# Kernel tuning notes

Hardware: AMD Instinct MI355X
Metric: run time of the kernel (lower is better)

Reference implementation:

```python
import jax, jax.numpy as jnp
import numpy as np

N_ATOMS = 100000
M_NBRS = 12
ATOM_F = 64
NBR_F = 41
BN_EPS = 1e-5


def setup_inputs() -> dict:
    key = jax.random.key(0)
    k1, k2, k3, k4, k5 = jax.random.split(key, 5)
    atom_fea = jax.random.normal(k1, (N_ATOMS, ATOM_F), dtype=jnp.float32)
    nbr_fea = jax.random.normal(k2, (N_ATOMS, M_NBRS, NBR_F), dtype=jnp.float32)
    # fc_full: Linear(2*atom + nbr -> 2*atom), torch layout [out, in]
    in_dim = 2 * ATOM_F + NBR_F
    out_dim = 2 * ATOM_F
    W = jax.random.normal(k3, (out_dim, in_dim), dtype=jnp.float32) * (1.0 / np.sqrt(in_dim))
    b = jax.random.normal(k4, (out_dim,), dtype=jnp.float32) * 0.01
    gamma = jnp.ones((ATOM_F,), dtype=jnp.float32)
    beta = jnp.zeros((ATOM_F,), dtype=jnp.float32)
    nbr_idx = jax.random.randint(k5, (N_ATOMS, M_NBRS), 0, N_ATOMS, dtype=jnp.int32)
    return {"atom_fea": atom_fea, "nbr_fea": nbr_fea, "W": W, "b": b,
            "gamma": gamma, "beta": beta, "nbr_idx": nbr_idx}


def reference(atom_fea, nbr_fea, W, b, gamma, beta, nbr_idx):
    N, M = nbr_idx.shape
    F = atom_fea.shape[1]
    # gather neighbor atom features: [N, M, F]
    nbr_atom_fea = atom_fea[nbr_idx]
    # broadcast self features: [N, M, F]
    self_fea = jnp.broadcast_to(atom_fea[:, None, :], (N, M, F))
    # concat [self, nbr_atom, edge] -> [N, M, 2F + nbr_F]
    total_fea = jnp.concatenate([self_fea, nbr_atom_fea, nbr_fea], axis=2)
    # shared linear: [N, M, 2F]
    total_fea = jnp.einsum('nmi,oi->nmo', total_fea, W) + b
    filter_fea, core_fea = jnp.split(total_fea, 2, axis=2)
    # gated message, sum over neighbors -> [N, F]
    nbr_msg = (jax.nn.sigmoid(filter_fea) * jax.nn.softplus(core_fea)).sum(axis=1)
    # BatchNorm1d (training mode: batch stats, biased variance)
    x = atom_fea + nbr_msg
    mean = x.mean(axis=0)
    var = x.var(axis=0)
    x_hat = (x - mean) * jax.lax.rsqrt(var + BN_EPS)
    out = x_hat * gamma + beta
    return jax.nn.softplus(out)
```

## Files before the change

kernel.cpp:

```cpp
#include <hip/hip_runtime.h>
#include <hip/hip_bf16.h>

#define N_ATOMS 100000
#define M_NBRS 12
#define ATOM_F 64
#define NBR_F 41
#define OUT_DIM 128
#define IN_DIM 169

typedef __attribute__((ext_vector_type(8))) short short8;
typedef __attribute__((ext_vector_type(4))) float f32x4;

__device__ __forceinline__ unsigned short f2bf(float f) {
    union { float f; unsigned u; } v; v.f = f;
    unsigned u = v.u;
    return (unsigned short)((u + 0x7fffu + ((u >> 16) & 1u)) >> 16);
}
__device__ __forceinline__ float bf2f(unsigned short h) {
    union { unsigned u; float f; } v; v.u = ((unsigned)h) << 16;
    return v.f;
}
__device__ __forceinline__ unsigned pack_bf2(float lo, float hi) {
    return (unsigned)f2bf(lo) | (((unsigned)f2bf(hi)) << 16);
}
__device__ __forceinline__ float softplus_f(float x) {
    return fmaxf(x, 0.f) + __logf(1.f + __expf(-fabsf(x)));
}
__device__ __forceinline__ float sigmoid_f(float x) {
    return 1.f / (1.f + __expf(-x));
}

#define WS_STRIDE 72
__global__ __launch_bounds__(256, 4) void k_prep(
    const float* __restrict__ atom, const float* __restrict__ W,
    const float* __restrict__ bias, unsigned* __restrict__ abf_u32,
    unsigned* __restrict__ A1u_out)
{
    __shared__ unsigned short Ws[128 * WS_STRIDE];
    __shared__ unsigned Ap[4 * 16 * 36];
    __shared__ unsigned short T1[4][16 * 136];
    const int tid = threadIdx.x;
    const int w = tid >> 6, l = tid & 63;
    const int r = l & 15, g = l >> 4;

    for (int e = tid; e < 128 * 64; e += 256) {
        int col = e >> 6, k = e & 63;
        Ws[col * WS_STRIDE + k] = f2bf(W[col * IN_DIM + k]);
    }
    __syncthreads();

    short8 bf[8][2];
    #pragma unroll
    for (int nt = 0; nt < 8; ++nt)
      #pragma unroll
      for (int kk = 0; kk < 2; ++kk) {
            int col = nt * 16 + r;
            union { uint4 u; short8 s; } u;
            u.u = *reinterpret_cast<const uint4*>(&Ws[col * WS_STRIDE + kk * 32 + g * 8]);
            bf[nt][kk] = u.s;
      }

    float bb[8];
    #pragma unroll
    for (int nt = 0; nt < 8; ++nt) bb[nt] = bias[nt * 16 + r];

    const int totalw = gridDim.x * 4;
    const int gw = blockIdx.x * 4 + w;
    const int step = totalw * 16;
    const int T = (N_ATOMS + step - 1) / step;
    unsigned* Aw = &Ap[w * 16 * 36];
    unsigned short* Tw = T1[w];

    for (int t = 0; t < T; ++t) {
        int base = gw * 16 + t * step;
        #pragma unroll
        for (int sub = 0; sub < 4; ++sub) {
            int chunk = g * 4 + sub;
            int a = base + r;
            float4 v = make_float4(0.f, 0.f, 0.f, 0.f);
            if (a < N_ATOMS)
                v = reinterpret_cast<const float4*>(atom)[a * 16 + chunk];
            Aw[r * 36 + chunk * 2]     = pack_bf2(v.x, v.y);
            Aw[r * 36 + chunk * 2 + 1] = pack_bf2(v.z, v.w);
        }
        {
            int al = l >> 2, part = l & 3;
            int a = base + al;
            if (a < N_ATOMS) {
                uint4 d0 = *reinterpret_cast<const uint4*>(&Aw[al * 36 + part * 8]);
                uint4 d1 = *reinterpret_cast<const uint4*>(&Aw[al * 36 + part * 8 + 4]);
                reinterpret_cast<uint4*>(&abf_u32[a * 32 + part * 8])[0] = d0;
                reinterpret_cast<uint4*>(&abf_u32[a * 32 + part * 8 + 4])[0] = d1;
            }
        }
        short8 af[2];
        #pragma unroll
        for (int kk = 0; kk < 2; ++kk) {
            union { uint4 u; short8 s; } u;
            u.u = *reinterpret_cast<const uint4*>(&Aw[r * 36 + kk * 16 + g * 4]);
            af[kk] = u.s;
        }
        #pragma unroll
        for (int nt = 0; nt < 8; ++nt) {
            f32x4 acc = {0.f, 0.f, 0.f, 0.f};
            acc = __builtin_amdgcn_mfma_f32_16x16x32_bf16(af[0], bf[nt][0], acc, 0, 0, 0);
            acc = __builtin_amdgcn_mfma_f32_16x16x32_bf16(af[1], bf[nt][1], acc, 0, 0, 0);
            int col = nt * 16 + r;
            #pragma unroll
            for (int r4 = 0; r4 < 4; ++r4) {
                int al = g * 4 + r4;
                Tw[al * 136 + col] = f2bf(acc[r4] + bb[nt]);
            }
        }
        {
            int al = l >> 2, part = l & 3;
            int a = base + al;
            if (a < N_ATOMS) {
                const unsigned* Twu = reinterpret_cast<const unsigned*>(&Tw[al * 136]);
                #pragma unroll
                for (int q = 0; q < 4; ++q) {
                    uint4 d = *reinterpret_cast<const uint4*>(&Twu[part * 16 + q * 4]);
                    reinterpret_cast<uint4*>(&A1u_out[a * 64 + part * 16 + q * 4])[0] = d;
                }
            }
        }
    }
}

struct Buf {
    unsigned ga[3], gb[3];
    float e0[3], e1[3], e2[3], e3[3];
    unsigned a1v;
    float av;
};

__device__ __forceinline__ Buf issue_loads(
    int i, bool act, unsigned idxv,
    const unsigned* __restrict__ abf_u32, const float* __restrict__ nbr,
    const unsigned* __restrict__ A1u, const float* __restrict__ atom,
    int c, int g, int l)
{
    Buf b;
    if (act) {
        #pragma unroll
        for (int rr = 0; rr < 3; ++rr) {
            int r = rr * 4 + g;
            int j = (int)__shfl(idxv, r, 64);
            b.ga[rr] = abf_u32[j * 32 + c];
            b.gb[rr] = abf_u32[j * 32 + 16 + c];
            int eb = (i * M_NBRS + r) * NBR_F;
            b.e0[rr] = nbr[eb + 2 * c];
            b.e1[rr] = nbr[eb + 2 * c + 1];
            b.e2[rr] = (c < 5) ? nbr[eb + 32 + 2 * c] : 0.f;
            b.e3[rr] = (c < 4) ? nbr[eb + 33 + 2 * c] : 0.f;
        }
        b.a1v = A1u[i * 64 + l];
        b.av  = atom[i * 64 + l];
    } else {
        #pragma unroll
        for (int rr = 0; rr < 3; ++rr) {
            b.ga[rr] = b.gb[rr] = 0u;
            b.e0[rr] = b.e1[rr] = b.e2[rr] = b.e3[rr] = 0.f;
        }
        b.a1v = 0u; b.av = 0.f;
    }
    return b;
}

#define BS_STRIDE 136
__global__ __launch_bounds__(256, 2) void k_msg(
    const float* __restrict__ atom, const float* __restrict__ nbr,
    const float* __restrict__ W, const int* __restrict__ idx,
    const unsigned* __restrict__ abf_u32, const unsigned* __restrict__ A1u,
    float* __restrict__ X)
{
    __shared__ unsigned short Bs[128 * BS_STRIDE];
    __shared__ unsigned Au[4 * 16 * 68];
    const int tid = threadIdx.x;
    const int w = tid >> 6, l = tid & 63;
    const int c = l & 15, g = l >> 4;
    unsigned* Aw = &Au[w * 16 * 68];

    for (int e = tid; e < 128 * BS_STRIDE / 2; e += 256)
        reinterpret_cast<unsigned*>(Bs)[e] = 0u;
    __syncthreads();
    for (int e = tid; e < 128 * 105; e += 256) {
        unsigned col = (unsigned)e / 105u;
        unsigned k = (unsigned)e - col * 105u;
        Bs[col * BS_STRIDE + k] = f2bf(W[col * IN_DIM + 64 + k]);
    }
    __syncthreads();

    short8 bf[8][4];
    #pragma unroll
    for (int nt = 0; nt < 8; ++nt)
      #pragma unroll
      for (int kk = 0; kk < 4; ++kk) {
            int col = nt * 16 + c;
            union { uint4 u; short8 s; } u;
            u.u = *reinterpret_cast<const uint4*>(&Bs[col * BS_STRIDE + kk * 32 + g * 8]);
            bf[nt][kk] = u.s;
      }

    for (int t = l; t < 4 * 68; t += 64)
        Aw[12 * 68 + t] = 0u;

    const int TW = gridDim.x * 4;
    const int gw = blockIdx.x * 4 + w;
    const int T = (N_ATOMS + TW - 1) / TW;

    int i0 = gw;
    bool act0 = (i0 < N_ATOMS);
    unsigned idxv0 = (l < 12 && act0) ? (unsigned)idx[i0 * M_NBRS + l] : 0u;
    Buf buf = issue_loads(i0, act0, idxv0, abf_u32, nbr, A1u, atom, c, g, l);
    int i1 = gw + TW;
    unsigned idxv_n = (l < 12 && i1 < N_ATOMS) ? (unsigned)idx[i1 * M_NBRS + l] : 0u;

    for (int t = 0; t < T; ++t) {
        int i = gw + t * TW;
        bool act = (i < N_ATOMS);
        int i_nxt = i + TW;
        bool act_n = (i_nxt < N_ATOMS);

        Buf buf_n = issue_loads(i_nxt, act_n, idxv_n, abf_u32, nbr, A1u, atom, c, g, l);
        int i_n2 = i + 2 * TW;
        unsigned idxv_n2 = (l < 12 && i_n2 < N_ATOMS) ? (unsigned)idx[i_n2 * M_NBRS + l] : 0u;

        if (act) {
            #pragma unroll
            for (int rr = 0; rr < 3; ++rr) {
                int r = rr * 4 + g;
                Aw[r * 68 + c]      = buf.ga[rr];
                Aw[r * 68 + 16 + c] = buf.gb[rr];
                Aw[r * 68 + 32 + c] = pack_bf2(buf.e0[rr], buf.e1[rr]);
                Aw[r * 68 + 48 + c] = (c < 5) ? pack_bf2(buf.e2[rr], buf.e3[rr]) : 0u;
            }
            short8 af[4];
            #pragma unroll
            for (int kk = 0; kk < 4; ++kk) {
                union { uint4 u; short8 s; } u;
                u.u = *reinterpret_cast<const uint4*>(&Aw[c * 68 + kk * 16 + g * 4]);
                af[kk] = u.s;
            }
            #pragma unroll
            for (int p = 0; p < 4; ++p) {
                f32x4 accf = {0.f,0.f,0.f,0.f}, accc = {0.f,0.f,0.f,0.f};
                #pragma unroll
                for (int kk = 0; kk < 4; ++kk) {
                    accf = __builtin_amdgcn_mfma_f32_16x16x32_bf16(af[kk], bf[p][kk],     accf, 0,0,0);
                    accc = __builtin_amdgcn_mfma_f32_16x16x32_bf16(af[kk], bf[p + 4][kk], accc, 0,0,0);
                }
                unsigned a1p = __shfl(buf.a1v, p * 8 + (c >> 1), 64);
                unsigned a1q = __shfl(buf.a1v, 32 + p * 8 + (c >> 1), 64);
                float a1f = bf2f((unsigned short)((c & 1) ? (a1p >> 16) : (a1p & 0xffffu)));
                float a1c = bf2f((unsigned short)((c & 1) ? (a1q >> 16) : (a1q & 0xffffu)));
                float ac  = __shfl(buf.av, p * 16 + c, 64);
                float gs = 0.f;
                if (g < 3) {
                    #pragma unroll
                    for (int r4 = 0; r4 < 4; ++r4) {
                        float zf = accf[r4] + a1f;
                        float zc = accc[r4] + a1c;
                        gs += sigmoid_f(zf) * softplus_f(zc);
                    }
                }
                gs += __shfl_xor(gs, 16, 64);
                gs += __shfl_xor(gs, 32, 64);
                if (g == 0)
                    X[i * ATOM_F + p * 16 + c] = ac + gs;
            }
        }
        buf = buf_n;
        idxv_n = idxv_n2;
    }
}

#define S1_BLOCKS 256
__global__ void k_stats1(const float* __restrict__ X, float* __restrict__ PART)
{
    __shared__ float s1[256], s2[256];
    int tid = threadIdx.x;
    int f = tid & 63;
    int seg = blockIdx.x * 4 + (tid >> 6);
    float sum = 0.f, sq = 0.f;
    for (int a = seg; a < N_ATOMS; a += S1_BLOCKS * 4) {
        float x = X[a * ATOM_F + f];
        sum += x; sq += x * x;
    }
    s1[tid] = sum; s2[tid] = sq;
    __syncthreads();
    if (tid < 64) {
        PART[blockIdx.x * 128 + tid] = s1[tid] + s1[tid+64] + s1[tid+128] + s1[tid+192];
    } else if (tid < 128) {
        int ff = tid - 64;
        PART[blockIdx.x * 128 + tid] = s2[ff] + s2[ff+64] + s2[ff+128] + s2[ff+192];
    }
}

__global__ void k_stats2(const float* __restrict__ PART, const float* __restrict__ gamma,
                         const float* __restrict__ beta, float* __restrict__ MS)
{
    __shared__ float st[128];
    int t = threadIdx.x;
    float s = 0.f;
    #pragma unroll 8
    for (int b = 0; b < S1_BLOCKS; ++b) s += PART[b * 128 + t];
    st[t] = s;
    __syncthreads();
    if (t < 64) {
        float mean = st[t] * (1.f / N_ATOMS);
        float msq  = st[64 + t] * (1.f / N_ATOMS);
        float var  = msq - mean * mean;
        float inv  = rsqrtf(var + 1e-5f);
        float sc   = inv * gamma[t];
        float sh   = beta[t] - mean * sc;
        MS[t] = sc;
        MS[64 + t] = sh;
    }
}

__global__ void k_final(float* __restrict__ X, const float* __restrict__ MS)
{
    int q = blockIdx.x * 256 + threadIdx.x;
    const float4* MS4 = reinterpret_cast<const float4*>(MS);
    float4 x = reinterpret_cast<const float4*>(X)[q];
    float4 sc = MS4[q & 15];
    float4 sh = MS4[16 + (q & 15)];
    float4 o;
    o.x = softplus_f(x.x * sc.x + sh.x);
    o.y = softplus_f(x.y * sc.y + sh.y);
    o.z = softplus_f(x.z * sc.z + sh.z);
    o.w = softplus_f(x.w * sc.w + sh.w);
    reinterpret_cast<float4*>(X)[q] = o;
}

extern "C" void kernel_launch(void* const* d_in, const int* in_sizes, int n_in,
                              void* d_out, int out_size, void* d_ws, size_t ws_size,
                              hipStream_t stream)
{
    const float* atom  = (const float*)d_in[0];
    const float* nbr   = (const float*)d_in[1];
    const float* W     = (const float*)d_in[2];
    const float* bias  = (const float*)d_in[3];
    const float* gamma = (const float*)d_in[4];
    const float* beta  = (const float*)d_in[5];
    const int*   idx   = (const int*)d_in[6];
    float* X = (float*)d_out;

    char* ws = (char*)d_ws;
    unsigned* abf = (unsigned*)ws;
    unsigned* A1u = (unsigned*)(ws + (size_t)N_ATOMS * 64 * 2);
    float* PART   = (float*)(ws + (size_t)N_ATOMS * 64 * 2
                                + (size_t)N_ATOMS * 128 * 2);
    float* MS     = PART + S1_BLOCKS * 128;

    hipLaunchKernelGGL(k_prep,   dim3(512),       dim3(256), 0, stream, atom, W, bias, abf, A1u);
    hipLaunchKernelGGL(k_msg,    dim3(512),       dim3(256), 0, stream, atom, nbr, W, idx, abf, A1u, X);
    hipLaunchKernelGGL(k_stats1, dim3(S1_BLOCKS), dim3(256), 0, stream, X, PART);
    hipLaunchKernelGGL(k_stats2, dim3(1),         dim3(128), 0, stream, PART, gamma, beta, MS);
    hipLaunchKernelGGL(k_final,  dim3(6250),      dim3(256), 0, stream, X, MS);
}
```

Baseline: 492.8 us.

## Tile message kernel over 16 atoms per neighbor slot and fuse batch-norm statistics

The message kernel now puts 16 atoms in the MFMA rows for one neighbor slot at a time, instead of the 12 neighbors of a single atom. Each wave walks all 12 slots, accumulates gated messages in registers and prefetches the next slot's gathers. Batch-norm sums and sums of squares are reduced inside the message kernel and combined with atomics, which removes the separate stats1 pass over X. The prep kernel stores the self-projection in an interleaved filter/core bf16 layout and uses hardware packed bf16 conversion. The trade-offs are float atomics with nondeterministic summation order and more register pressure.

Measured after the change: 721.2 us. +46.3%, slower.

```diff
diff --git a/kernel.cpp b/kernel.cpp
--- a/kernel.cpp
+++ b/kernel.cpp
@@ -1,5 +1,4 @@
 #include <hip/hip_runtime.h>
-#include <hip/hip_bf16.h>
 
 #define N_ATOMS 100000
 #define M_NBRS 12
@@ -7,41 +6,44 @@
 #define NBR_F 41
 #define OUT_DIM 128
 #define IN_DIM 169
+#define N_GROUPS (N_ATOMS / 16)
 
 typedef __attribute__((ext_vector_type(8))) short short8;
 typedef __attribute__((ext_vector_type(4))) float f32x4;
+typedef __attribute__((ext_vector_type(2))) unsigned u32x2;
+typedef __attribute__((ext_vector_type(4))) unsigned u32x4;
 
 __device__ __forceinline__ unsigned short f2bf(float f) {
     union { float f; unsigned u; } v; v.f = f;
     unsigned u = v.u;
     return (unsigned short)((u + 0x7fffu + ((u >> 16) & 1u)) >> 16);
 }
-__device__ __forceinline__ float bf2f(unsigned short h) {
-    union { unsigned u; float f; } v; v.u = ((unsigned)h) << 16;
-    return v.f;
-}
-__device__ __forceinline__ unsigned pack_bf2(float lo, float hi) {
-    return (unsigned)f2bf(lo) | (((unsigned)f2bf(hi)) << 16);
+__device__ __forceinline__ unsigned cvt_pk(float a, float b) {
+    unsigned r;
+    asm("v_cvt_pk_bf16_f32 %0, %1, %2" : "=v"(r) : "v"(a), "v"(b));
+    return r;
 }
 __device__ __forceinline__ float softplus_f(float x) {
     return fmaxf(x, 0.f) + __logf(1.f + __expf(-fabsf(x)));
 }
 __device__ __forceinline__ float sigmoid_f(float x) {
-    return 1.f / (1.f + __expf(-x));
+    return __fdividef(1.f, 1.f + __expf(-x));
 }
 
 #define WS_STRIDE 72
 __global__ __launch_bounds__(256, 4) void k_prep(
     const float* __restrict__ atom, const float* __restrict__ W,
     const float* __restrict__ bias, unsigned* __restrict__ abf_u32,
-    unsigned* __restrict__ A1u_out)
+    unsigned* __restrict__ A1P, float* __restrict__ SUM)
 {
     __shared__ unsigned short Ws[128 * WS_STRIDE];
     __shared__ unsigned Ap[4 * 16 * 36];
-    __shared__ unsigned short T1[4][16 * 136];
+    __shared__ unsigned T2[4][16 * 68];
     const int tid = threadIdx.x;
     const int w = tid >> 6, l = tid & 63;
     const int r = l & 15, g = l >> 4;
+
+    if (blockIdx.x == 0 && tid < 128) SUM[tid] = 0.f;
 
     for (int e = tid; e < 128 * 64; e += 256) {
         int col = e >> 6, k = e & 63;
@@ -55,11 +57,10 @@
       #pragma unroll
       for (int kk = 0; kk < 2; ++kk) {
             int col = nt * 16 + r;
-            union { uint4 u; short8 s; } u;
-            u.u = *reinterpret_cast<const uint4*>(&Ws[col * WS_STRIDE + kk * 32 + g * 8]);
+            union { u32x4 u; short8 s; } u;
+            u.u = *reinterpret_cast<const u32x4*>(&Ws[col * WS_STRIDE + kk * 32 + g * 8]);
             bf[nt][kk] = u.s;
       }
-
     float bb[8];
     #pragma unroll
     for (int nt = 0; nt < 8; ++nt) bb[nt] = bias[nt * 16 + r];
@@ -69,7 +70,7 @@
     const int step = totalw * 16;
     const int T = (N_ATOMS + step - 1) / step;
     unsigned* Aw = &Ap[w * 16 * 36];
-    unsigned short* Tw = T1[w];
+    unsigned* Tw = T2[w];
 
     for (int t = 0; t < T; ++t) {
         int base = gw * 16 + t * step;
@@ -80,106 +81,86 @@
             float4 v = make_float4(0.f, 0.f, 0.f, 0.f);
             if (a < N_ATOMS)
                 v = reinterpret_cast<const float4*>(atom)[a * 16 + chunk];
-            Aw[r * 36 + chunk * 2]     = pack_bf2(v.x, v.y);
-            Aw[r * 36 + chunk * 2 + 1] = pack_bf2(v.z, v.w);
+            Aw[r * 36 + chunk * 2]     = cvt_pk(v.x, v.y);
+            Aw[r * 36 + chunk * 2 + 1] = cvt_pk(v.z, v.w);
         }
         {
             int al = l >> 2, part = l & 3;
             int a = base + al;
             if (a < N_ATOMS) {
-                uint4 d0 = *reinterpret_cast<const uint4*>(&Aw[al * 36 + part * 8]);
-                uint4 d1 = *reinterpret_cast<const uint4*>(&Aw[al * 36 + part * 8 + 4]);
-                reinterpret_cast<uint4*>(&abf_u32[a * 32 + part * 8])[0] = d0;
-                reinterpret_cast<uint4*>(&abf_u32[a * 32 + part * 8 + 4])[0] = d1;
+                u32x4 d0 = *reinterpret_cast<const u32x4*>(&Aw[al * 36 + part * 8]);
+                u32x4 d1 = *reinterpret_cast<const u32x4*>(&Aw[al * 36 + part * 8 + 4]);
+                *reinterpret_cast<u32x4*>(&abf_u32[(size_t)a * 32 + part * 8]) = d0;
+                *reinterpret_cast<u32x4*>(&abf_u32[(size_t)a * 32 + part * 8 + 4]) = d1;
             }
         }
         short8 af[2];
         #pragma unroll
         for (int kk = 0; kk < 2; ++kk) {
-            union { uint4 u; short8 s; } u;
-            u.u = *reinterpret_cast<const uint4*>(&Aw[r * 36 + kk * 16 + g * 4]);
+            union { u32x4 u; short8 s; } u;
+            u.u = *reinterpret_cast<const u32x4*>(&Aw[r * 36 + kk * 16 + g * 4]);
             af[kk] = u.s;
         }
         #pragma unroll
-        for (int nt = 0; nt < 8; ++nt) {
-            f32x4 acc = {0.f, 0.f, 0.f, 0.f};
-            acc = __builtin_amdgcn_mfma_f32_16x16x32_bf16(af[0], bf[nt][0], acc, 0, 0, 0);
-            acc = __builtin_amdgcn_mfma_f32_16x16x32_bf16(af[1], bf[nt][1], acc, 0, 0, 0);
-            int col = nt * 16 + r;
+        for (int nt = 0; nt < 4; ++nt) {
+            f32x4 accf = {0.f,0.f,0.f,0.f}, accc = {0.f,0.f,0.f,0.f};
+            accf = __builtin_amdgcn_mfma_f32_16x16x32_bf16(af[0], bf[nt][0],   accf, 0,0,0);
+            accf = __builtin_amdgcn_mfma_f32_16x16x32_bf16(af[1], bf[nt][1],   accf, 0,0,0);
+            accc = __builtin_amdgcn_mfma_f32_16x16x32_bf16(af[0], bf[nt+4][0], accc, 0,0,0);
+            accc = __builtin_amdgcn_mfma_f32_16x16x32_bf16(af[1], bf[nt+4][1], accc, 0,0,0);
             #pragma unroll
             for (int r4 = 0; r4 < 4; ++r4) {
-                int al = g * 4 + r4;
-                Tw[al * 136 + col] = f2bf(acc[r4] + bb[nt]);
+                int row = g * 4 + r4;
+                Tw[row * 68 + r * 4 + nt] = cvt_pk(accf[r4] + bb[nt], accc[r4] + bb[nt + 4]);
             }
         }
         {
             int al = l >> 2, part = l & 3;
             int a = base + al;
             if (a < N_ATOMS) {
-                const unsigned* Twu = reinterpret_cast<const unsigned*>(&Tw[al * 136]);
                 #pragma unroll
                 for (int q = 0; q < 4; ++q) {
-                    uint4 d = *reinterpret_cast<const uint4*>(&Twu[part * 16 + q * 4]);
-                    reinterpret_cast<uint4*>(&A1u_out[a * 64 + part * 16 + q * 4])[0] = d;
+                    u32x4 d = *reinterpret_cast<const u32x4*>(&Tw[al * 68 + part * 16 + q * 4]);
+                    *reinterpret_cast<u32x4*>(&A1P[(size_t)a * 64 + part * 16 + q * 4]) = d;
                 }
             }
         }
     }
 }
 
-struct Buf {
-    unsigned ga[3], gb[3];
-    float e0[3], e1[3], e2[3], e3[3];
-    unsigned a1v;
-    float av;
-};
-
-__device__ __forceinline__ Buf issue_loads(
-    int i, bool act, unsigned idxv,
-    const unsigned* __restrict__ abf_u32, const float* __restrict__ nbr,
-    const unsigned* __restrict__ A1u, const float* __restrict__ atom,
-    int c, int g, int l)
-{
-    Buf b;
-    if (act) {
-        #pragma unroll
-        for (int rr = 0; rr < 3; ++rr) {
-            int r = rr * 4 + g;
-            int j = (int)__shfl(idxv, r, 64);
-            b.ga[rr] = abf_u32[j * 32 + c];
-            b.gb[rr] = abf_u32[j * 32 + 16 + c];
-            int eb = (i * M_NBRS + r) * NBR_F;
-            b.e0[rr] = nbr[eb + 2 * c];
-            b.e1[rr] = nbr[eb + 2 * c + 1];
-            b.e2[rr] = (c < 5) ? nbr[eb + 32 + 2 * c] : 0.f;
-            b.e3[rr] = (c < 4) ? nbr[eb + 33 + 2 * c] : 0.f;
-        }
-        b.a1v = A1u[i * 64 + l];
-        b.av  = atom[i * 64 + l];
-    } else {
-        #pragma unroll
-        for (int rr = 0; rr < 3; ++rr) {
-            b.ga[rr] = b.gb[rr] = 0u;
-            b.e0[rr] = b.e1[rr] = b.e2[rr] = b.e3[rr] = 0.f;
-        }
-        b.a1v = 0u; b.av = 0.f;
+#define BS_STRIDE 136
+
+struct TBuf { u32x2 ga[4]; float f0[4], f1[4], f2[4], f3[4]; };
+
+__device__ __forceinline__ TBuf load_data(
+    const unsigned* __restrict__ abf, const float* __restrict__ nbr,
+    int base, int m, const int* jj, int c, int g)
+{
+    TBuf b;
+    #pragma unroll
+    for (int rr = 0; rr < 4; ++rr) {
+        b.ga[rr] = *reinterpret_cast<const u32x2*>(abf + (size_t)jj[rr] * 32 + 2 * c);
+        const float* ep = nbr + ((size_t)(base + rr * 4 + g) * M_NBRS + m) * NBR_F + 4 * c;
+        bool c10 = (c < 10);
+        b.f0[rr] = (c < 11) ? ep[0] : 0.f;
+        b.f1[rr] = c10 ? ep[1] : 0.f;
+        b.f2[rr] = c10 ? ep[2] : 0.f;
+        b.f3[rr] = c10 ? ep[3] : 0.f;
     }
     return b;
 }
 
-#define BS_STRIDE 136
 __global__ __launch_bounds__(256, 2) void k_msg(
     const float* __restrict__ atom, const float* __restrict__ nbr,
     const float* __restrict__ W, const int* __restrict__ idx,
-    const unsigned* __restrict__ abf_u32, const unsigned* __restrict__ A1u,
-    float* __restrict__ X)
-{
-    __shared__ unsigned short Bs[128 * BS_STRIDE];
-    __shared__ unsigned Au[4 * 16 * 68];
+    const unsigned* __restrict__ abf, const unsigned* __restrict__ A1P,
+    float* __restrict__ X, float* __restrict__ SUM)
+{
+    __shared__ __align__(16) unsigned short Bs[128 * BS_STRIDE];
     const int tid = threadIdx.x;
     const int w = tid >> 6, l = tid & 63;
     const int c = l & 15, g = l >> 4;
-    unsigned* Aw = &Au[w * 16 * 68];
+    unsigned* Aw = reinterpret_cast<unsigned*>(Bs) + w * 16 * 68;
 
     for (int e = tid; e < 128 * BS_STRIDE / 2; e += 256)
         reinterpret_cast<unsigned*>(Bs)[e] = 0u;
@@ -197,49 +178,68 @@
       #pragma unroll
       for (int kk = 0; kk < 4; ++kk) {
             int col = nt * 16 + c;
-            union { uint4 u; short8 s; } u;
-            u.u = *reinterpret_cast<const uint4*>(&Bs[col * BS_STRIDE + kk * 32 + g * 8]);
+            union { u32x4 u; short8 s; } u;
+            u.u = *reinterpret_cast<const u32x4*>(&Bs[col * BS_STRIDE + kk * 32 + g * 8]);
             bf[nt][kk] = u.s;
       }
-
-    for (int t = l; t < 4 * 68; t += 64)
-        Aw[12 * 68 + t] = 0u;
+    __syncthreads();
 
     const int TW = gridDim.x * 4;
     const int gw = blockIdx.x * 4 + w;
-    const int T = (N_ATOMS + TW - 1) / TW;
-
-    int i0 = gw;
-    bool act0 = (i0 < N_ATOMS);
-    unsigned idxv0 = (l < 12 && act0) ? (unsigned)idx[i0 * M_NBRS + l] : 0u;
-    Buf buf = issue_loads(i0, act0, idxv0, abf_u32, nbr, A1u, atom, c, g, l);
-    int i1 = gw + TW;
-    unsigned idxv_n = (l < 12 && i1 < N_ATOMS) ? (unsigned)idx[i1 * M_NBRS + l] : 0u;
-
-    for (int t = 0; t < T; ++t) {
-        int i = gw + t * TW;
-        bool act = (i < N_ATOMS);
-        int i_nxt = i + TW;
-        bool act_n = (i_nxt < N_ATOMS);
-
-        Buf buf_n = issue_loads(i_nxt, act_n, idxv_n, abf_u32, nbr, A1u, atom, c, g, l);
-        int i_n2 = i + 2 * TW;
-        unsigned idxv_n2 = (l < 12 && i_n2 < N_ATOMS) ? (unsigned)idx[i_n2 * M_NBRS + l] : 0u;
-
-        if (act) {
-            #pragma unroll
-            for (int rr = 0; rr < 3; ++rr) {
+    float sum_p[4] = {0.f,0.f,0.f,0.f}, sq_p[4] = {0.f,0.f,0.f,0.f};
+
+    #pragma unroll 1
+    for (int grp = gw; grp < N_GROUPS; grp += TW) {
+        const int base = grp * 16;
+        u32x4 a1q[4];
+        #pragma unroll
+        for (int r4 = 0; r4 < 4; ++r4)
+            a1q[r4] = *reinterpret_cast<const u32x4*>(
+                &A1P[(size_t)(base + g * 4 + r4) * 64 + c * 4]);
+
+        float gs[4][4];
+        #pragma unroll
+        for (int r4 = 0; r4 < 4; ++r4)
+          #pragma unroll
+          for (int p = 0; p < 4; ++p) gs[r4][p] = 0.f;
+
+        int jn[4];
+        TBuf buf;
+        {
+            int j0[4];
+            #pragma unroll
+            for (int rr = 0; rr < 4; ++rr)
+                j0[rr] = idx[(base + rr * 4 + g) * M_NBRS + 0];
+            buf = load_data(abf, nbr, base, 0, j0, c, g);
+        }
+        #pragma unroll
+        for (int rr = 0; rr < 4; ++rr)
+            jn[rr] = idx[(base + rr * 4 + g) * M_NBRS + 1];
+
+        #pragma unroll 4
+        for (int m = 0; m < M_NBRS; ++m) {
+            #pragma unroll
+            for (int rr = 0; rr < 4; ++rr) {
                 int r = rr * 4 + g;
-                Aw[r * 68 + c]      = buf.ga[rr];
-                Aw[r * 68 + 16 + c] = buf.gb[rr];
-                Aw[r * 68 + 32 + c] = pack_bf2(buf.e0[rr], buf.e1[rr]);
-                Aw[r * 68 + 48 + c] = (c < 5) ? pack_bf2(buf.e2[rr], buf.e3[rr]) : 0u;
+                *reinterpret_cast<u32x2*>(Aw + r * 68 + 2 * c) = buf.ga[rr];
+                u32x2 e;
+                e[0] = cvt_pk(buf.f0[rr], buf.f1[rr]);
+                e[1] = cvt_pk(buf.f2[rr], buf.f3[rr]);
+                *reinterpret_cast<u32x2*>(Aw + r * 68 + 32 + 2 * c) = e;
+            }
+            if (m + 1 < M_NBRS) {
+                buf = load_data(abf, nbr, base, m + 1, jn, c, g);
+                if (m + 2 < M_NBRS) {
+                    #pragma unroll
+                    for (int rr = 0; rr < 4; ++rr)
+                        jn[rr] = idx[(base + rr * 4 + g) * M_NBRS + m + 2];
+                }
             }
             short8 af[4];
             #pragma unroll
             for (int kk = 0; kk < 4; ++kk) {
-                union { uint4 u; short8 s; } u;
-                u.u = *reinterpret_cast<const uint4*>(&Aw[c * 68 + kk * 16 + g * 4]);
+                union { u32x4 u; short8 s; } u;
+                u.u = *reinterpret_cast<const u32x4*>(&Aw[c * 68 + kk * 16 + g * 4]);
                 af[kk] = u.s;
             }
             #pragma unroll
@@ -250,73 +250,65 @@
                     accf = __builtin_amdgcn_mfma_f32_16x16x32_bf16(af[kk], bf[p][kk],     accf, 0,0,0);
                     accc = __builtin_amdgcn_mfma_f32_16x16x32_bf16(af[kk], bf[p + 4][kk], accc, 0,0,0);
                 }
-                unsigned a1p = __shfl(buf.a1v, p * 8 + (c >> 1), 64);
-                unsigned a1q = __shfl(buf.a1v, 32 + p * 8 + (c >> 1), 64);
-                float a1f = bf2f((unsigned short)((c & 1) ? (a1p >> 16) : (a1p & 0xffffu)));
-                float a1c = bf2f((unsigned short)((c & 1) ? (a1q >> 16) : (a1q & 0xffffu)));
-                float ac  = __shfl(buf.av, p * 16 + c, 64);
-                float gs = 0.f;
-                if (g < 3) {
-                    #pragma unroll
-                    for (int r4 = 0; r4 < 4; ++r4) {
-                        float zf = accf[r4] + a1f;
-                        float zc = accc[r4] + a1c;
-                        gs += sigmoid_f(zf) * softplus_f(zc);
-                    }
+                #pragma unroll
+                for (int r4 = 0; r4 < 4; ++r4) {
+                    unsigned a1 = a1q[r4][p];
+                    float zf = accf[r4] + __uint_as_float(a1 << 16);
+                    float zc = accc[r4] + __uint_as_float(a1 & 0xffff0000u);
+                    gs[r4][p] += sigmoid_f(zf) * softplus_f(zc);
                 }
-                gs += __shfl_xor(gs, 16, 64);
-                gs += __shfl_xor(gs, 32, 64);
-                if (g == 0)
-                    X[i * ATOM_F + p * 16 + c] = ac + gs;
-            }
-        }
-        buf = buf_n;
-        idxv_n = idxv_n2;
-    }
-}
-
-#define S1_BLOCKS 256
-__global__ void k_stats1(const float* __restrict__ X, float* __restrict__ PART)
-{
-    __shared__ float s1[256], s2[256];
-    int tid = threadIdx.x;
-    int f = tid & 63;
-    int seg = blockIdx.x * 4 + (tid >> 6);
-    float sum = 0.f, sq = 0.f;
-    for (int a = seg; a < N_ATOMS; a += S1_BLOCKS * 4) {
-        float x = X[a * ATOM_F + f];
-        sum += x; sq += x * x;
-    }
-    s1[tid] = sum; s2[tid] = sq;
-    __syncthreads();
-    if (tid < 64) {
-        PART[blockIdx.x * 128 + tid] = s1[tid] + s1[tid+64] + s1[tid+128] + s1[tid+192];
-    } else if (tid < 128) {
-        int ff = tid - 64;
-        PART[blockIdx.x * 128 + tid] = s2[ff] + s2[ff+64] + s2[ff+128] + s2[ff+192];
-    }
-}
-
-__global__ void k_stats2(const float* __restrict__ PART, const float* __restrict__ gamma,
+            }
+        }
+        #pragma unroll
+        for (int r4 = 0; r4 < 4; ++r4) {
+            int o = (base + g * 4 + r4) * ATOM_F + c;
+            #pragma unroll
+            for (int p = 0; p < 4; ++p) {
+                float x = atom[o + p * 16] + gs[r4][p];
+                X[o + p * 16] = x;
+                sum_p[p] += x;
+                sq_p[p] += x * x;
+            }
+        }
+    }
+
+    #pragma unroll
+    for (int p = 0; p < 4; ++p) {
+        sum_p[p] += __shfl_xor(sum_p[p], 16, 64);
+        sum_p[p] += __shfl_xor(sum_p[p], 32, 64);
+        sq_p[p]  += __shfl_xor(sq_p[p], 16, 64);
+        sq_p[p]  += __shfl_xor(sq_p[p], 32, 64);
+    }
+    __syncthreads();
+    float* Rs = reinterpret_cast<float*>(Bs);
+    if (g == 0) {
+        #pragma unroll
+        for (int p = 0; p < 4; ++p) {
+            Rs[w * 128 + p * 16 + c] = sum_p[p];
+            Rs[512 + w * 128 + p * 16 + c] = sq_p[p];
+        }
+    }
+    __syncthreads();
+    if (tid < 128) {
+        int q = tid & 63;
+        int o = (tid >> 6) * 512;
+        float v = Rs[o + q] + Rs[o + 128 + q] + Rs[o + 256 + q] + Rs[o + 384 + q];
+        atomicAdd(&SUM[tid], v);
+    }
+}
+
+__global__ void k_stats2(const float* __restrict__ SUM, const float* __restrict__ gamma,
                          const float* __restrict__ beta, float* __restrict__ MS)
 {
-    __shared__ float st[128];
     int t = threadIdx.x;
-    float s = 0.f;
-    #pragma unroll 8
-    for (int b = 0; b < S1_BLOCKS; ++b) s += PART[b * 128 + t];
-    st[t] = s;
-    __syncthreads();
-    if (t < 64) {
-        float mean = st[t] * (1.f / N_ATOMS);
-        float msq  = st[64 + t] * (1.f / N_ATOMS);
-        float var  = msq - mean * mean;
-        float inv  = rsqrtf(var + 1e-5f);
-        float sc   = inv * gamma[t];
-        float sh   = beta[t] - mean * sc;
-        MS[t] = sc;
-        MS[64 + t] = sh;
-    }
+    float mean = SUM[t] * (1.f / N_ATOMS);
+    float msq  = SUM[64 + t] * (1.f / N_ATOMS);
+    float var  = msq - mean * mean;
+    float inv  = rsqrtf(var + 1e-5f);
+    float sc   = inv * gamma[t];
+    float sh   = beta[t] - mean * sc;
+    MS[t] = sc;
+    MS[64 + t] = sh;
 }
 
 __global__ void k_final(float* __restrict__ X, const float* __restrict__ MS)
@@ -349,14 +341,13 @@
 
     char* ws = (char*)d_ws;
     unsigned* abf = (unsigned*)ws;
-    unsigned* A1u = (unsigned*)(ws + (size_t)N_ATOMS * 64 * 2);
-    float* PART   = (float*)(ws + (size_t)N_ATOMS * 64 * 2
-                                + (size_t)N_ATOMS * 128 * 2);
-    float* MS     = PART + S1_BLOCKS * 128;
-
-    hipLaunchKernelGGL(k_prep,   dim3(512),       dim3(256), 0, stream, atom, W, bias, abf, A1u);
-    hipLaunchKernelGGL(k_msg,    dim3(512),       dim3(256), 0, stream, atom, nbr, W, idx, abf, A1u, X);
-    hipLaunchKernelGGL(k_stats1, dim3(S1_BLOCKS), dim3(256), 0, stream, X, PART);
-    hipLaunchKernelGGL(k_stats2, dim3(1),         dim3(128), 0, stream, PART, gamma, beta, MS);
-    hipLaunchKernelGGL(k_final,  dim3(6250),      dim3(256), 0, stream, X, MS);
-}
+    unsigned* A1P = (unsigned*)(ws + (size_t)N_ATOMS * 32 * 4);
+    float* SUM    = (float*)(ws + (size_t)N_ATOMS * 32 * 4
+                                + (size_t)N_ATOMS * 64 * 4);
+    float* MS     = SUM + 128;
+
+    hipLaunchKernelGGL(k_prep,   dim3(512),  dim3(256), 0, stream, atom, W, bias, abf, A1P, SUM);
+    hipLaunchKernelGGL(k_msg,    dim3(512),  dim3(256), 0, stream, atom, nbr, W, idx, abf, A1P, X, SUM);
+    hipLaunchKernelGGL(k_stats2, dim3(1),    dim3(64),  0, stream, SUM, gamma, beta, MS);
+    hipLaunchKernelGGL(k_final,  dim3(6250), dim3(256), 0, stream, X, MS);
+}
```
